# Kernel tuning notes

Measured on AMD Instinct MI355X. Metric: run time of the kernel, lower is better.

## Reference

```python
import jax, jax.numpy as jnp
import numpy as np

B, D, DP, H = 65536, 512, 256, 8
HD = D // H  # head dim = 64
EPS = 1e-5


def _layernorm(x, gamma, beta):
    mu = jnp.mean(x, axis=-1, keepdims=True)
    var = jnp.var(x, axis=-1, keepdims=True)
    return (x - mu) * jax.lax.rsqrt(var + EPS) * gamma + beta


def setup_inputs() -> dict:
    key = jax.random.key(0)
    ks = jax.random.split(key, 16)
    n = lambda k, shape, s=0.02: (jax.random.normal(k, shape, jnp.float32) * s)
    return {
        "cell_emb": jax.random.normal(ks[0], (B, D), jnp.float32),
        "pert_emb": jax.random.normal(ks[1], (B, DP), jnp.float32),
        # perturbation_proj: Linear(DP -> D)
        "Wp": n(ks[2], (D, DP)), "bp": jnp.zeros((D,), jnp.float32),
        # MultiheadAttention in/out projections (each D x D)
        "Wq": n(ks[3], (D, D)), "bq": jnp.zeros((D,), jnp.float32),
        "Wk": n(ks[4], (D, D)), "bk": jnp.zeros((D,), jnp.float32),
        "Wv": n(ks[5], (D, D)), "bv": jnp.zeros((D,), jnp.float32),
        "Wo": n(ks[6], (D, D)), "bo": jnp.zeros((D,), jnp.float32),
        # norm1, norm2
        "g1": jnp.ones((D,), jnp.float32), "be1": jnp.zeros((D,), jnp.float32),
        "g2": jnp.ones((D,), jnp.float32), "be2": jnp.zeros((D,), jnp.float32),
        # FFN: Linear(D -> 2D), GELU, Linear(2D -> D)
        "W1": n(ks[7], (2 * D, D)), "b1": jnp.zeros((2 * D,), jnp.float32),
        "W2": n(ks[8], (D, 2 * D)), "b2": jnp.zeros((D,), jnp.float32),
    }


def reference(cell_emb, pert_emb, Wp, bp, Wq, bq, Wk, bk, Wv, bv, Wo, bo,
              g1, be1, g2, be2, W1, b1, W2, b2):
    # kv = perturbation_proj(pert_emb), length-1 KV sequence
    kv = pert_emb @ Wp.T + bp                       # (B, D)
    # MultiheadAttention with q_len = kv_len = 1
    q = (cell_emb @ Wq.T + bq).reshape(B, H, HD)    # (B, H, HD)
    k = (kv @ Wk.T + bk).reshape(B, H, HD)
    v = (kv @ Wv.T + bv).reshape(B, H, HD)
    # scores over a single key -> softmax yields 1, kept for faithfulness
    logits = jnp.sum(q * k, axis=-1, keepdims=True) / jnp.sqrt(jnp.float32(HD))  # (B, H, 1)
    w = jax.nn.softmax(logits, axis=-1)             # == ones (single key)
    attn = (w * v).reshape(B, D)
    attn_out = attn @ Wo.T + bo                     # (B, D)
    x = _layernorm(cell_emb + attn_out, g1, be1)
    # FFN with exact (erf) GELU, matching torch nn.GELU default
    h = jax.nn.gelu(x @ W1.T + b1, approximate=False)
    ffn_out = h @ W2.T + b2
    return _layernorm(x + ffn_out, g2, be2)
```

## Files before the change

### kernel.cpp

```cpp
#include <hip/hip_runtime.h>
#include <hip/hip_bf16.h>

typedef __bf16 bf16_t;
typedef __attribute__((ext_vector_type(8))) __bf16 bf16x8;
typedef __attribute__((ext_vector_type(4))) float f32x4;

__global__ void prep_wvp(const float* __restrict__ Wv, const float* __restrict__ Wp,
                         const float* __restrict__ bp, const float* __restrict__ bv,
                         float* __restrict__ Wvp, float* __restrict__ bvp) {
  const int i = blockIdx.x;
  const int j = threadIdx.x;
  float a = 0.f;
  for (int d = 0; d < 512; ++d) a += Wv[i * 512 + d] * Wp[d * 256 + j];
  Wvp[i * 256 + j] = a;
  if (j == 0) {
    float b = 0.f;
    for (int d = 0; d < 512; ++d) b += Wv[i * 512 + d] * bp[d];
    bvp[i] = b + bv[i];
  }
}

__global__ void prep_wc(const float* __restrict__ Wo, const float* __restrict__ bo,
                        const float* __restrict__ Wvp, const float* __restrict__ bvp,
                        bf16_t* __restrict__ Wc, float* __restrict__ bcomb) {
  const int o = blockIdx.x;
  const int j = threadIdx.x;
  float a = 0.f;
  for (int i = 0; i < 512; ++i) a += Wo[o * 512 + i] * Wvp[i * 256 + j];
  const int g = o >> 4, rr = o & 15, t = j >> 5, q = (j >> 3) & 3, e = j & 7;
  Wc[((((size_t)g * 8 + t) * 64) + q * 16 + rr) * 8 + e] = (bf16_t)a;
  if (j == 0) {
    float b = 0.f;
    for (int i = 0; i < 512; ++i) b += Wo[o * 512 + i] * bvp[i];
    bcomb[o] = b + bo[o];
  }
}

__global__ void prep_cast(const float* __restrict__ W1, const float* __restrict__ W2,
                          bf16_t* __restrict__ W1b, bf16_t* __restrict__ W2b) {
  const int idx = (blockIdx.x * 256 + threadIdx.x) * 8;
  const float* s;
  bf16_t* d;
  if (idx < 524288) {
    const int o = idx >> 9, k = idx & 511;
    const int g = o >> 4, rr = o & 15, t = k >> 5, q = (k >> 3) & 3;
    s = W1 + idx;
    d = W1b + ((((size_t)g * 16 + t) * 64) + q * 16 + rr) * 8;
  } else {
    const int i2 = idx - 524288;
    const int o = i2 >> 10, k = i2 & 1023;
    const int g = o >> 4, rr = o & 15, t = k >> 5, q = (k >> 3) & 3;
    s = W2 + i2;
    d = W2b + ((((size_t)g * 32 + t) * 64) + q * 16 + rr) * 8;
  }
  float4 u0 = *(const float4*)s;
  float4 u1 = *(const float4*)(s + 4);
  bf16x8 v;
  v[0] = (bf16_t)u0.x; v[1] = (bf16_t)u0.y; v[2] = (bf16_t)u0.z; v[3] = (bf16_t)u0.w;
  v[4] = (bf16_t)u1.x; v[5] = (bf16_t)u1.y; v[6] = (bf16_t)u1.z; v[7] = (bf16_t)u1.w;
  *(bf16x8*)d = v;
}


__device__ __forceinline__ int alay(int row, int k) {
  const int rr = row & 15;
  const int c = (k >> 3) & 3;
  return ((k >> 5) * 4 + (row >> 4)) * 512 +
         (rr * 4 + (c ^ ((rr >> 1) & 3))) * 8 + (k & 7);
}

template <int STEPS, int NJ>
__device__ __forceinline__ void kloop(const bf16_t* __restrict__ lA_,
                                      const bf16_t* __restrict__ Bp,
                                      int g0, int SB, int soff,
                                      int fRd, int lane,
                                      f32x4 (&acc)[4][NJ]) {
  auto bfrag = [&](int j, int s) {
    return *(const bf16x8*)(Bp + ((size_t)((g0 + j) * SB + (soff + s)) * 64 + lane) * 8);
  };
  bf16x8 bCur[NJ], bNxt[NJ];
#pragma unroll
  for (int j = 0; j < NJ; ++j) bCur[j] = bfrag(j, 0);
#pragma unroll
  for (int s = 0; s < STEPS; ++s) {
    bf16x8 af[4];
#pragma unroll
    for (int i = 0; i < 4; ++i) af[i] = *(const bf16x8*)&lA_[(s * 4 + i) * 512 + fRd];
    if (s + 1 < STEPS) {
#pragma unroll
      for (int j = 0; j < NJ; ++j) bNxt[j] = bfrag(j, s + 1);
    }
    __builtin_amdgcn_s_setprio(1);
#pragma unroll
    for (int j = 0; j < NJ; ++j)
#pragma unroll
      for (int i = 0; i < 4; ++i)
        acc[i][j] = __builtin_amdgcn_mfma_f32_16x16x32_bf16(af[i], bCur[j], acc[i][j], 0, 0, 0);
    __builtin_amdgcn_s_setprio(0);
#pragma unroll
    for (int j = 0; j < NJ; ++j) bCur[j] = bNxt[j];
  }
}

__global__ __launch_bounds__(256, 2) void fused_block(
    const float* __restrict__ pert, const bf16_t* __restrict__ Wc,
    const float* __restrict__ bcomb, const float* __restrict__ cell,
    const float* __restrict__ g1, const float* __restrict__ be1,
    const bf16_t* __restrict__ W1b, const float* __restrict__ b1,
    const bf16_t* __restrict__ W2b, const float* __restrict__ b2,
    const float* __restrict__ g2, const float* __restrict__ be2,
    float* __restrict__ out) {

  __shared__ __align__(16) bf16_t lX[64 * 512];
  __shared__ __align__(16) bf16_t lH[64 * 128];
  float* rsP = (float*)lH;
  float* ssP = (float*)lH + 256;

  const int t = threadIdx.x;
  const int m0 = blockIdx.x * 64;
  const int lane = t & 63;
  const int wc = t >> 6;
  const int r = lane & 15;
  const int q = lane >> 4;
  const int qs = q ^ ((r >> 1) & 3);
  const int fRd = r * 32 + qs * 8;

#pragma unroll
  for (int u = 0; u < 8; ++u) {
    const int g = u * 256 + t;
    const int row = g >> 5;
    const int c = g & 31;
    const float* src = pert + (size_t)(m0 + row) * 256 + c * 8;
    float4 u0 = *(const float4*)src;
    float4 u1 = *(const float4*)(src + 4);
    bf16x8 v;
    v[0] = (bf16_t)u0.x; v[1] = (bf16_t)u0.y; v[2] = (bf16_t)u0.z; v[3] = (bf16_t)u0.w;
    v[4] = (bf16_t)u1.x; v[5] = (bf16_t)u1.y; v[6] = (bf16_t)u1.z; v[7] = (bf16_t)u1.w;
    *(bf16x8*)&lX[alay(row, c * 8)] = v;
  }
  __syncthreads();

  {
    f32x4 acc1[4][8];
#pragma unroll
    for (int i = 0; i < 4; ++i)
#pragma unroll
      for (int j = 0; j < 8; ++j)
#pragma unroll
        for (int p = 0; p < 4; ++p) acc1[i][j][p] = 0.f;
    kloop<8, 8>(lX, Wc, 8 * wc, 8, 0, fRd, lane, acc1);

    float s_[4][4], ss_[4][4];
#pragma unroll
    for (int i = 0; i < 4; ++i)
#pragma unroll
      for (int p = 0; p < 4; ++p) { s_[i][p] = 0.f; ss_[i][p] = 0.f; }
    float bb[8];
#pragma unroll
    for (int j = 0; j < 8; ++j) bb[j] = bcomb[128 * wc + 16 * j + r];
#pragma unroll
    for (int i = 0; i < 4; ++i)
#pragma unroll
      for (int p = 0; p < 4; ++p) {
        const int rowl = 16 * i + 4 * q + p;
#pragma unroll
        for (int j = 0; j < 8; ++j) {
          const int col = 128 * wc + 16 * j + r;
          float v = acc1[i][j][p] + bb[j] + cell[(size_t)(m0 + rowl) * 512 + col];
          acc1[i][j][p] = v;
          s_[i][p] += v;
          ss_[i][p] += v * v;
        }
      }
#pragma unroll
    for (int m = 1; m <= 8; m <<= 1)
#pragma unroll
      for (int i = 0; i < 4; ++i)
#pragma unroll
        for (int p = 0; p < 4; ++p) {
          s_[i][p] += __shfl_xor(s_[i][p], m);
          ss_[i][p] += __shfl_xor(ss_[i][p], m);
        }
    __syncthreads();
    if (r == 0) {
#pragma unroll
      for (int i = 0; i < 4; ++i)
#pragma unroll
        for (int p = 0; p < 4; ++p) {
          const int rowl = 16 * i + 4 * q + p;
          rsP[wc * 64 + rowl] = s_[i][p];
          ssP[wc * 64 + rowl] = ss_[i][p];
        }
    }
    __syncthreads();
    float mu[4][4], inv[4][4];
#pragma unroll
    for (int i = 0; i < 4; ++i)
#pragma unroll
      for (int p = 0; p < 4; ++p) {
        const int rowl = 16 * i + 4 * q + p;
        float tS = rsP[rowl] + rsP[64 + rowl] + rsP[128 + rowl] + rsP[192 + rowl];
        float tQ = ssP[rowl] + ssP[64 + rowl] + ssP[128 + rowl] + ssP[192 + rowl];
        float m_ = tS * (1.0f / 512.0f);
        float v_ = tQ * (1.0f / 512.0f) - m_ * m_;
        mu[i][p] = m_;
        inv[i][p] = rsqrtf(v_ + 1e-5f);
      }
    float ga[8], be[8];
#pragma unroll
    for (int j = 0; j < 8; ++j) {
      ga[j] = g1[128 * wc + 16 * j + r];
      be[j] = be1[128 * wc + 16 * j + r];
    }
#pragma unroll
    for (int i = 0; i < 4; ++i)
#pragma unroll
      for (int p = 0; p < 4; ++p) {
        const int rowl = 16 * i + 4 * q + p;
#pragma unroll
        for (int j = 0; j < 8; ++j) {
          const int col = 128 * wc + 16 * j + r;
          float v = (acc1[i][j][p] - mu[i][p]) * inv[i][p] * ga[j] + be[j];
          lX[alay(rowl, col)] = (bf16_t)v;
        }
      }
  }
  __syncthreads();

  f32x4 acc3[4][8];
#pragma unroll
  for (int i = 0; i < 4; ++i)
#pragma unroll
    for (int j = 0; j < 8; ++j)
#pragma unroll
      for (int p = 0; p < 4; ++p) acc3[i][j][p] = 0.f;

  for (int e = 0; e < 8; ++e) {
    {
      f32x4 accq[4][2];
#pragma unroll
      for (int i = 0; i < 4; ++i)
#pragma unroll
        for (int j = 0; j < 2; ++j)
#pragma unroll
          for (int p = 0; p < 4; ++p) accq[i][j][p] = 0.f;
      kloop<16, 2>(lX, W1b, 8 * e + 2 * wc, 16, 0, fRd, lane, accq);
      float bb1[2];
#pragma unroll
      for (int j = 0; j < 2; ++j) bb1[j] = b1[128 * e + 32 * wc + 16 * j + r];
#pragma unroll
      for (int i = 0; i < 4; ++i)
#pragma unroll
        for (int p = 0; p < 4; ++p) {
          const int rowl = 16 * i + 4 * q + p;
#pragma unroll
          for (int j = 0; j < 2; ++j) {
            const int col = 32 * wc + 16 * j + r;
            float v = accq[i][j][p] + bb1[j];
            float g = 0.5f * v * (1.0f + erff(v * 0.70710678118654752f));
            lH[alay(rowl, col)] = (bf16_t)g;
          }
        }
    }
    __syncthreads();
    kloop<4, 8>(lH, W2b, 8 * wc, 32, 4 * e, fRd, lane, acc3);
    __syncthreads();
  }

  {
    float s_[4][4], ss_[4][4];
#pragma unroll
    for (int i = 0; i < 4; ++i)
#pragma unroll
      for (int p = 0; p < 4; ++p) { s_[i][p] = 0.f; ss_[i][p] = 0.f; }
    float bb2[8];
#pragma unroll
    for (int j = 0; j < 8; ++j) bb2[j] = b2[128 * wc + 16 * j + r];
#pragma unroll
    for (int i = 0; i < 4; ++i)
#pragma unroll
      for (int p = 0; p < 4; ++p) {
        const int rowl = 16 * i + 4 * q + p;
#pragma unroll
        for (int j = 0; j < 8; ++j) {
          const int col = 128 * wc + 16 * j + r;
          float v = acc3[i][j][p] + bb2[j] + (float)lX[alay(rowl, col)];
          acc3[i][j][p] = v;
          s_[i][p] += v;
          ss_[i][p] += v * v;
        }
      }
#pragma unroll
    for (int m = 1; m <= 8; m <<= 1)
#pragma unroll
      for (int i = 0; i < 4; ++i)
#pragma unroll
        for (int p = 0; p < 4; ++p) {
          s_[i][p] += __shfl_xor(s_[i][p], m);
          ss_[i][p] += __shfl_xor(ss_[i][p], m);
        }
    if (r == 0) {
#pragma unroll
      for (int i = 0; i < 4; ++i)
#pragma unroll
        for (int p = 0; p < 4; ++p) {
          const int rowl = 16 * i + 4 * q + p;
          rsP[wc * 64 + rowl] = s_[i][p];
          ssP[wc * 64 + rowl] = ss_[i][p];
        }
    }
    __syncthreads();
    float mu[4][4], inv[4][4];
#pragma unroll
    for (int i = 0; i < 4; ++i)
#pragma unroll
      for (int p = 0; p < 4; ++p) {
        const int rowl = 16 * i + 4 * q + p;
        float tS = rsP[rowl] + rsP[64 + rowl] + rsP[128 + rowl] + rsP[192 + rowl];
        float tQ = ssP[rowl] + ssP[64 + rowl] + ssP[128 + rowl] + ssP[192 + rowl];
        float m_ = tS * (1.0f / 512.0f);
        float v_ = tQ * (1.0f / 512.0f) - m_ * m_;
        mu[i][p] = m_;
        inv[i][p] = rsqrtf(v_ + 1e-5f);
      }
    float ga[8], be[8];
#pragma unroll
    for (int j = 0; j < 8; ++j) {
      ga[j] = g2[128 * wc + 16 * j + r];
      be[j] = be2[128 * wc + 16 * j + r];
    }
#pragma unroll
    for (int i = 0; i < 4; ++i)
#pragma unroll
      for (int p = 0; p < 4; ++p) {
        const int rowl = 16 * i + 4 * q + p;
#pragma unroll
        for (int j = 0; j < 8; ++j) {
          const int col = 128 * wc + 16 * j + r;
          out[(size_t)(m0 + rowl) * 512 + col] =
              (acc3[i][j][p] - mu[i][p]) * inv[i][p] * ga[j] + be[j];
        }
      }
  }
}

extern "C" void kernel_launch(void* const* d_in, const int* in_sizes, int n_in,
                              void* d_out, int out_size, void* d_ws, size_t ws_size,
                              hipStream_t stream) {
  const float* cell = (const float*)d_in[0];
  const float* pert = (const float*)d_in[1];
  const float* Wp   = (const float*)d_in[2];
  const float* bp   = (const float*)d_in[3];
  const float* Wv   = (const float*)d_in[8];
  const float* bv   = (const float*)d_in[9];
  const float* Wo   = (const float*)d_in[10];
  const float* bo   = (const float*)d_in[11];
  const float* g1   = (const float*)d_in[12];
  const float* be1  = (const float*)d_in[13];
  const float* g2   = (const float*)d_in[14];
  const float* be2  = (const float*)d_in[15];
  const float* W1   = (const float*)d_in[16];
  const float* b1   = (const float*)d_in[17];
  const float* W2   = (const float*)d_in[18];
  const float* b2   = (const float*)d_in[19];

  char* ws = (char*)d_ws;
  float*  Wvp   = (float*)(ws + 0);
  float*  bvp   = (float*)(ws + 524288);
  float*  bcomb = (float*)(ws + 526336);
  bf16_t* Wc    = (bf16_t*)(ws + 528384);
  bf16_t* W1b   = (bf16_t*)(ws + 790528);
  bf16_t* W2b   = (bf16_t*)(ws + 1839104);
  (void)in_sizes; (void)n_in; (void)out_size; (void)ws_size;

  prep_wvp<<<512, 256, 0, stream>>>(Wv, Wp, bp, bv, Wvp, bvp);
  prep_wc<<<512, 256, 0, stream>>>(Wo, bo, Wvp, bvp, Wc, bcomb);
  prep_cast<<<512, 256, 0, stream>>>(W1, W2, W1b, W2b);

  fused_block<<<1024, 256, 0, stream>>>(pert, Wc, bcomb, cell, g1, be1,
                                        W1b, b1, W2b, b2, g2, be2,
                                        (float*)d_out);
}
```

Before: 602.5 us.

## Split B-fragment prefetch into halves and merge weight-prep kernels

Rewrites the two weight-folding prep kernels so each thread computes four output columns with float4 loads and a wave-shuffle bias reduction. The Wo·Wvp fold and the W1/W2 bf16 cast now run in one launch, cutting a kernel launch. The MFMA inner loop now loads B fragments in two halves: the second half loads while the first half's MFMAs run, which lowers live registers compared with holding full current and next buffers. The price is a shorter prefetch distance for the second half.

Result: slower. 617.6 us (+2.5%).

```diff
diff --git a/kernel.cpp b/kernel.cpp
--- a/kernel.cpp
+++ b/kernel.cpp
@@ -5,60 +5,87 @@
 typedef __attribute__((ext_vector_type(8))) __bf16 bf16x8;
 typedef __attribute__((ext_vector_type(4))) float f32x4;
 
-__global__ void prep_wvp(const float* __restrict__ Wv, const float* __restrict__ Wp,
-                         const float* __restrict__ bp, const float* __restrict__ bv,
-                         float* __restrict__ Wvp, float* __restrict__ bvp) {
-  const int i = blockIdx.x;
-  const int j = threadIdx.x;
-  float a = 0.f;
-  for (int d = 0; d < 512; ++d) a += Wv[i * 512 + d] * Wp[d * 256 + j];
-  Wvp[i * 256 + j] = a;
-  if (j == 0) {
-    float b = 0.f;
-    for (int d = 0; d < 512; ++d) b += Wv[i * 512 + d] * bp[d];
-    bvp[i] = b + bv[i];
-  }
-}
-
-__global__ void prep_wc(const float* __restrict__ Wo, const float* __restrict__ bo,
-                        const float* __restrict__ Wvp, const float* __restrict__ bvp,
-                        bf16_t* __restrict__ Wc, float* __restrict__ bcomb) {
-  const int o = blockIdx.x;
-  const int j = threadIdx.x;
-  float a = 0.f;
-  for (int i = 0; i < 512; ++i) a += Wo[o * 512 + i] * Wvp[i * 256 + j];
-  const int g = o >> 4, rr = o & 15, t = j >> 5, q = (j >> 3) & 3, e = j & 7;
-  Wc[((((size_t)g * 8 + t) * 64) + q * 16 + rr) * 8 + e] = (bf16_t)a;
-  if (j == 0) {
-    float b = 0.f;
-    for (int i = 0; i < 512; ++i) b += Wo[o * 512 + i] * bvp[i];
-    bcomb[o] = b + bo[o];
-  }
-}
-
-__global__ void prep_cast(const float* __restrict__ W1, const float* __restrict__ W2,
-                          bf16_t* __restrict__ W1b, bf16_t* __restrict__ W2b) {
-  const int idx = (blockIdx.x * 256 + threadIdx.x) * 8;
-  const float* s;
-  bf16_t* d;
-  if (idx < 524288) {
-    const int o = idx >> 9, k = idx & 511;
-    const int g = o >> 4, rr = o & 15, t = k >> 5, q = (k >> 3) & 3;
-    s = W1 + idx;
-    d = W1b + ((((size_t)g * 16 + t) * 64) + q * 16 + rr) * 8;
+__global__ __launch_bounds__(256) void prep_wvp_fast(
+    const float* __restrict__ Wv, const float* __restrict__ Wp,
+    const float* __restrict__ bp, const float* __restrict__ bv,
+    float* __restrict__ Wvp, float* __restrict__ bvp) {
+  const int t = threadIdx.x;
+  const int rs = t >> 6;
+  const int jg = t & 63;
+  const int i = blockIdx.x * 4 + rs;
+  const float* wrow = Wv + (size_t)i * 512;
+  float4 acc = {0.f, 0.f, 0.f, 0.f};
+#pragma unroll 4
+  for (int d = 0; d < 512; ++d) {
+    const float s = wrow[d];
+    const float4 p = *(const float4*)&Wp[d * 256 + jg * 4];
+    acc.x += s * p.x; acc.y += s * p.y; acc.z += s * p.z; acc.w += s * p.w;
+  }
+  *(float4*)&Wvp[(size_t)i * 256 + jg * 4] = acc;
+  float pb = 0.f;
+#pragma unroll
+  for (int u = 0; u < 8; ++u) { const int d = jg * 8 + u; pb += wrow[d] * bp[d]; }
+#pragma unroll
+  for (int m = 1; m <= 32; m <<= 1) pb += __shfl_xor(pb, m);
+  if (jg == 0) bvp[i] = pb + bv[i];
+}
+
+__global__ __launch_bounds__(256) void prep_wc_cast(
+    const float* __restrict__ Wo, const float* __restrict__ bo,
+    const float* __restrict__ Wvp, const float* __restrict__ bvp,
+    bf16_t* __restrict__ Wc, float* __restrict__ bcomb,
+    const float* __restrict__ W1, const float* __restrict__ W2,
+    bf16_t* __restrict__ W1b, bf16_t* __restrict__ W2b) {
+  const int b = blockIdx.x;
+  const int t = threadIdx.x;
+  if (b < 128) {
+    const int rs = t >> 6, jg = t & 63;
+    const int o = b * 4 + rs;
+    const float* worow = Wo + (size_t)o * 512;
+    float4 acc = {0.f, 0.f, 0.f, 0.f};
+#pragma unroll 4
+    for (int i = 0; i < 512; ++i) {
+      const float s = worow[i];
+      const float4 p = *(const float4*)&Wvp[i * 256 + jg * 4];
+      acc.x += s * p.x; acc.y += s * p.y; acc.z += s * p.z; acc.w += s * p.w;
+    }
+    const int g = o >> 4, rr = o & 15;
+    const float av[4] = {acc.x, acc.y, acc.z, acc.w};
+#pragma unroll
+    for (int u = 0; u < 4; ++u) {
+      const int k = jg * 4 + u;
+      const int tt = k >> 5, q = (k >> 3) & 3, e = k & 7;
+      Wc[((((size_t)g * 8 + tt) * 64) + q * 16 + rr) * 8 + e] = (bf16_t)av[u];
+    }
+    float pb = 0.f;
+#pragma unroll
+    for (int u = 0; u < 8; ++u) { const int i = jg * 8 + u; pb += worow[i] * bvp[i]; }
+#pragma unroll
+    for (int m = 1; m <= 32; m <<= 1) pb += __shfl_xor(pb, m);
+    if (jg == 0) bcomb[o] = pb + bo[o];
   } else {
-    const int i2 = idx - 524288;
-    const int o = i2 >> 10, k = i2 & 1023;
-    const int g = o >> 4, rr = o & 15, t = k >> 5, q = (k >> 3) & 3;
-    s = W2 + i2;
-    d = W2b + ((((size_t)g * 32 + t) * 64) + q * 16 + rr) * 8;
-  }
-  float4 u0 = *(const float4*)s;
-  float4 u1 = *(const float4*)(s + 4);
-  bf16x8 v;
-  v[0] = (bf16_t)u0.x; v[1] = (bf16_t)u0.y; v[2] = (bf16_t)u0.z; v[3] = (bf16_t)u0.w;
-  v[4] = (bf16_t)u1.x; v[5] = (bf16_t)u1.y; v[6] = (bf16_t)u1.z; v[7] = (bf16_t)u1.w;
-  *(bf16x8*)d = v;
+    const int idx = ((b - 128) * 256 + t) * 8;
+    const float* s;
+    bf16_t* d;
+    if (idx < 524288) {
+      const int o = idx >> 9, k = idx & 511;
+      const int g = o >> 4, rr = o & 15, tt = k >> 5, q = (k >> 3) & 3;
+      s = W1 + idx;
+      d = W1b + ((((size_t)g * 16 + tt) * 64) + q * 16 + rr) * 8;
+    } else {
+      const int i2 = idx - 524288;
+      const int o = i2 >> 10, k = i2 & 1023;
+      const int g = o >> 4, rr = o & 15, tt = k >> 5, q = (k >> 3) & 3;
+      s = W2 + i2;
+      d = W2b + ((((size_t)g * 32 + tt) * 64) + q * 16 + rr) * 8;
+    }
+    float4 u0 = *(const float4*)s;
+    float4 u1 = *(const float4*)(s + 4);
+    bf16x8 v;
+    v[0] = (bf16_t)u0.x; v[1] = (bf16_t)u0.y; v[2] = (bf16_t)u0.z; v[3] = (bf16_t)u0.w;
+    v[4] = (bf16_t)u1.x; v[5] = (bf16_t)u1.y; v[6] = (bf16_t)u1.z; v[7] = (bf16_t)u1.w;
+    *(bf16x8*)d = v;
+  }
 }
 
 
@@ -75,30 +102,38 @@
                                       int g0, int SB, int soff,
                                       int fRd, int lane,
                                       f32x4 (&acc)[4][NJ]) {
+  constexpr int H = NJ / 2;
   auto bfrag = [&](int j, int s) {
     return *(const bf16x8*)(Bp + ((size_t)((g0 + j) * SB + (soff + s)) * 64 + lane) * 8);
   };
-  bf16x8 bCur[NJ], bNxt[NJ];
-#pragma unroll
-  for (int j = 0; j < NJ; ++j) bCur[j] = bfrag(j, 0);
+  bf16x8 bA[H], bB[H];
+#pragma unroll
+  for (int j = 0; j < H; ++j) bA[j] = bfrag(j, 0);
 #pragma unroll
   for (int s = 0; s < STEPS; ++s) {
+#pragma unroll
+    for (int j = 0; j < H; ++j) bB[j] = bfrag(H + j, s);
     bf16x8 af[4];
 #pragma unroll
     for (int i = 0; i < 4; ++i) af[i] = *(const bf16x8*)&lA_[(s * 4 + i) * 512 + fRd];
+    __builtin_amdgcn_s_setprio(1);
+#pragma unroll
+    for (int j = 0; j < H; ++j)
+#pragma unroll
+      for (int i = 0; i < 4; ++i)
+        acc[i][j] = __builtin_amdgcn_mfma_f32_16x16x32_bf16(af[i], bA[j], acc[i][j], 0, 0, 0);
+    __builtin_amdgcn_s_setprio(0);
     if (s + 1 < STEPS) {
 #pragma unroll
-      for (int j = 0; j < NJ; ++j) bNxt[j] = bfrag(j, s + 1);
+      for (int j = 0; j < H; ++j) bA[j] = bfrag(j, s + 1);
     }
     __builtin_amdgcn_s_setprio(1);
 #pragma unroll
-    for (int j = 0; j < NJ; ++j)
-#pragma unroll
-      for (int i = 0; i < 4; ++i)
-        acc[i][j] = __builtin_amdgcn_mfma_f32_16x16x32_bf16(af[i], bCur[j], acc[i][j], 0, 0, 0);
+    for (int j = 0; j < H; ++j)
+#pragma unroll
+      for (int i = 0; i < 4; ++i)
+        acc[i][H + j] = __builtin_amdgcn_mfma_f32_16x16x32_bf16(af[i], bB[j], acc[i][H + j], 0, 0, 0);
     __builtin_amdgcn_s_setprio(0);
-#pragma unroll
-    for (int j = 0; j < NJ; ++j) bCur[j] = bNxt[j];
   }
 }
 
@@ -373,9 +408,9 @@
   bf16_t* W2b   = (bf16_t*)(ws + 1839104);
   (void)in_sizes; (void)n_in; (void)out_size; (void)ws_size;
 
-  prep_wvp<<<512, 256, 0, stream>>>(Wv, Wp, bp, bv, Wvp, bvp);
-  prep_wc<<<512, 256, 0, stream>>>(Wo, bo, Wvp, bvp, Wc, bcomb);
-  prep_cast<<<512, 256, 0, stream>>>(W1, W2, W1b, W2b);
+  prep_wvp_fast<<<128, 256, 0, stream>>>(Wv, Wp, bp, bv, Wvp, bvp);
+  prep_wc_cast<<<640, 256, 0, stream>>>(Wo, bo, Wvp, bvp, Wc, bcomb,
+                                        W1, W2, W1b, W2b);
 
   fused_block<<<1024, 256, 0, stream>>>(pert, Wc, bcomb, cell, g1, be1,
                                         W1b, b1, W2b, b2, g2, be2,
```
